# Kernel tuning notes

Hardware: AMD Instinct MI355X
Metric: run time of the kernel (lower is better)

The kernel has to match this reference:

```python
import jax, jax.numpy as jnp
import numpy as np

U = 128  # linear_units

def setup_inputs() -> dict:
    key = jax.random.key(0)
    k1, k2, k3, k4, k5, k6 = jax.random.split(key, 6)
    B, S, D = 16, 2048, 128
    x = jax.random.normal(k1, (B, S, D), dtype=jnp.float32)
    t = jax.random.uniform(k2, (B, S), dtype=jnp.float32)
    # glorot_uniform inits
    lim_qk = np.sqrt(6.0 / (D + U)).astype(np.float32)
    Wq = jax.random.uniform(k3, (D, U), minval=-lim_qk, maxval=lim_qk, dtype=jnp.float32)
    Wk = jax.random.uniform(k4, (D, U), minval=-lim_qk, maxval=lim_qk, dtype=jnp.float32)
    lim_s = np.sqrt(6.0 / (1 + S)).astype(np.float32)
    theta = jax.random.uniform(k5, (1, S), minval=-lim_s, maxval=lim_s, dtype=jnp.float32)
    mu = jax.random.uniform(k6, (1, S), minval=-lim_s, maxval=lim_s, dtype=jnp.float32)
    return {"x": x, "t": t, "Wq": Wq, "Wk": Wk, "theta": theta, "mu": mu}

def reference(x, t, Wq, Wk, theta, mu):
    # x: (B,S,D), t: (B,S), theta/mu: (1,S)
    scale = jnp.sqrt(jnp.asarray(U, dtype=x.dtype))
    q = x @ Wq                                   # (B,S,U)
    k = x @ Wk                                   # (B,S,U)
    scores = jnp.einsum('biu,bju->bij', q, k) / scale  # (B,S,S)
    alphas = jax.nn.softmax(scores, axis=-1)
    gn = jnp.einsum('bij,bjd->bid', alphas, x)   # weighted sum == alphas @ x, (B,S,D)
    time_fact = jax.nn.sigmoid(theta - mu * t)   # (B,S)
    v = jnp.sum(gn * time_fact[:, :, None], axis=1)  # (B,D)
    return v
```

## Files before the change

kernel.cpp:

```cpp
#include <hip/hip_runtime.h>
#include <hip/hip_bf16.h>

#define SS 2048
#define DD 128
#define BB 16
#define LDST 136
#define SCT 268

typedef short bf16x8 __attribute__((ext_vector_type(8)));
typedef float f32x4 __attribute__((ext_vector_type(4)));
typedef unsigned short ushort_t;

__device__ __forceinline__ unsigned short f2bf(float f) {
  union { float f; unsigned u; } v; v.f = f;
  unsigned r = v.u + 0x7fffu + ((v.u >> 16) & 1u);
  return (unsigned short)(r >> 16);
}
__device__ __forceinline__ float fexp2(float x) { return __builtin_amdgcn_exp2f(x); }


__global__ __launch_bounds__(256) void wprep(
    const float* __restrict__ Wq, const float* __restrict__ Wk,
    ushort_t* __restrict__ wt_g) {
  int idx = blockIdx.x * 256 + threadIdx.x;
  int r = idx & 16383, uu = r >> 7, d = r & 127;
  if (idx < 16384)
    wt_g[uu * 128 + d] = f2bf(Wq[d * 128 + uu] * 0.1275174346f);
  else
    wt_g[(uu + 128) * 128 + d] = f2bf(Wk[d * 128 + uu]);
}

__global__ __launch_bounds__(256, 2) void qk_gemm(
    const float* __restrict__ x, const ushort_t* __restrict__ wt_g,
    uint4* __restrict__ qF, uint4* __restrict__ kF) {
  __shared__ ushort_t xs[64 * LDST];
  __shared__ ushort_t sc[64 * SCT];
  const int tid = threadIdx.x, wave = tid >> 6, lane = tid & 63;
  const int lq = lane & 15, quad = lane >> 4;
  const int m0 = blockIdx.x * 64;

#pragma unroll
  for (int i = 0; i < 8; ++i) {
    int idx = i * 256 + tid;
    int row = idx >> 5, c4 = (idx & 31) * 4;
    const float4 v = *(const float4*)(x + (size_t)(m0 + row) * DD + c4);
    ushort4 h;
    h.x = f2bf(v.x); h.y = f2bf(v.y); h.z = f2bf(v.z); h.w = f2bf(v.w);
    *(ushort4*)(&xs[row * LDST + c4]) = h;
  }
  bf16x8 wf[4][4];
#pragma unroll
  for (int nt = 0; nt < 4; ++nt)
#pragma unroll
    for (int ks = 0; ks < 4; ++ks)
      wf[nt][ks] = *(const bf16x8*)(wt_g + (wave * 64 + nt * 16 + lq) * 128 + ks * 32 + quad * 8);
  __syncthreads();

  f32x4 acc[4][4];
#pragma unroll
  for (int mt = 0; mt < 4; ++mt)
#pragma unroll
    for (int nt = 0; nt < 4; ++nt) acc[mt][nt] = (f32x4){0.f, 0.f, 0.f, 0.f};
#pragma unroll
  for (int mt = 0; mt < 4; ++mt) {
    bf16x8 af[4];
#pragma unroll
    for (int ks = 0; ks < 4; ++ks)
      af[ks] = *(const bf16x8*)(&xs[(mt * 16 + lq) * LDST + ks * 32 + quad * 8]);
#pragma unroll
    for (int nt = 0; nt < 4; ++nt)
#pragma unroll
      for (int ks = 0; ks < 4; ++ks)
        acc[mt][nt] = __builtin_amdgcn_mfma_f32_16x16x32_bf16(af[ks], wf[nt][ks], acc[mt][nt], 0, 0, 0);
  }
#pragma unroll
  for (int mt = 0; mt < 4; ++mt)
#pragma unroll
    for (int nt = 0; nt < 4; ++nt)
#pragma unroll
      for (int r = 0; r < 4; ++r)
        sc[(mt * 16 + quad * 4 + r) * SCT + wave * 64 + nt * 16 + lq] = f2bf(acc[mt][nt][r]);
  __syncthreads();
#pragma unroll
  for (int i = 0; i < 8; ++i) {
    int c = i * 256 + tid;
    int lane_c = c & 63, ks_c = (c >> 6) & 3, g_c = (c >> 8) & 3, isk = c >> 10;
    int li = lane_c & 15, qd = lane_c >> 4;
    int col = isk * 128 + ks_c * 32 + qd * 8;
    uint4 v = *(const uint4*)(&sc[(g_c * 16 + li) * SCT + col]);
    size_t G = (size_t)blockIdx.x * 4 + g_c;
    uint4* dst = isk ? kF : qF;
    dst[(G * 4 + ks_c) * 64 + lane_c] = v;
  }
}

__global__ __launch_bounds__(256, 2) void attn_fused(
    const uint4* __restrict__ qF, const uint4* __restrict__ kF,
    const float* __restrict__ t, const float* __restrict__ theta,
    const float* __restrict__ mu, float* __restrict__ w) {
  const int b = blockIdx.x >> 5;
  const int ib = blockIdx.x & 31;
  const int i0 = ib * 64;
  const int tid = threadIdx.x, wave = tid >> 6, lane = tid & 63;
  const int lq = lane & 15, quad = lane >> 4;

  __shared__ float rs_lds[4][64];
  __shared__ float c_lds[64];

  const bf16x8* qc = (const bf16x8*)qF;
  const bf16x8* kc = (const bf16x8*)kF;

  bf16x8 af[4][4];
#pragma unroll
  for (int mt = 0; mt < 4; ++mt)
#pragma unroll
    for (int ks = 0; ks < 4; ++ks)
      af[mt][ks] = qc[((size_t)(b * 128 + ib * 4 + mt) * 4 + ks) * 64 + lane];

  bf16x8 cur[2][4], nxt[2][4];
  auto load_tile = [&](bf16x8 (&f)[2][4], int jt) {
#pragma unroll
    for (int nt = 0; nt < 2; ++nt) {
      int gg = jt * 8 + wave * 2 + nt;
#pragma unroll
      for (int ks = 0; ks < 4; ++ks)
        f[nt][ks] = kc[((size_t)(b * 128 + gg) * 4 + ks) * 64 + lane];
    }
  };

  float rowsum[4][4];
#pragma unroll
  for (int mt = 0; mt < 4; ++mt)
#pragma unroll
    for (int r = 0; r < 4; ++r) rowsum[mt][r] = 0.f;

  auto compute_p1 = [&](bf16x8 (&f)[2][4]) {
#pragma unroll
    for (int nt = 0; nt < 2; ++nt) {
      f32x4 acc[4];
#pragma unroll
      for (int mt = 0; mt < 4; ++mt) acc[mt] = (f32x4){0.f, 0.f, 0.f, 0.f};
#pragma unroll
      for (int ks = 0; ks < 4; ++ks)
#pragma unroll
        for (int mt = 0; mt < 4; ++mt)
          acc[mt] = __builtin_amdgcn_mfma_f32_16x16x32_bf16(af[mt][ks], f[nt][ks], acc[mt], 0, 0, 0);
#pragma unroll
      for (int mt = 0; mt < 4; ++mt)
#pragma unroll
        for (int r = 0; r < 4; ++r) rowsum[mt][r] += fexp2(acc[mt][r]);
    }
  };

  load_tile(cur, 0);
  for (int jt = 0; jt < 16; jt += 2) {
    load_tile(nxt, jt + 1);
    compute_p1(cur);
    if (jt + 2 < 16) load_tile(cur, jt + 2);
    compute_p1(nxt);
  }

#pragma unroll
  for (int d2 = 1; d2 <= 8; d2 <<= 1)
#pragma unroll
    for (int mt = 0; mt < 4; ++mt)
#pragma unroll
      for (int r = 0; r < 4; ++r)
        rowsum[mt][r] += __shfl_xor(rowsum[mt][r], d2, 64);
  if (lq == 0) {
#pragma unroll
    for (int mt = 0; mt < 4; ++mt)
#pragma unroll
      for (int r = 0; r < 4; ++r)
        rs_lds[wave][mt * 16 + quad * 4 + r] = rowsum[mt][r];
  }
  __syncthreads();
  if (tid < 64) {
    float l = rs_lds[0][tid] + rs_lds[1][tid] + rs_lds[2][tid] + rs_lds[3][tid];
    int gi = i0 + tid;
    float z = theta[gi] - mu[gi] * t[b * SS + gi];
    float tf = 1.f / (1.f + fexp2(-z * 1.44269504f));
    c_lds[tid] = tf / l;
  }
  __syncthreads();
  float creg[4][4];
#pragma unroll
  for (int mt = 0; mt < 4; ++mt)
#pragma unroll
    for (int r = 0; r < 4; ++r) creg[mt][r] = c_lds[mt * 16 + quad * 4 + r];

  auto compute_p2 = [&](bf16x8 (&f)[2][4], int jt) {
#pragma unroll
    for (int nt = 0; nt < 2; ++nt) {
      f32x4 acc[4];
#pragma unroll
      for (int mt = 0; mt < 4; ++mt) acc[mt] = (f32x4){0.f, 0.f, 0.f, 0.f};
#pragma unroll
      for (int ks = 0; ks < 4; ++ks)
#pragma unroll
        for (int mt = 0; mt < 4; ++mt)
          acc[mt] = __builtin_amdgcn_mfma_f32_16x16x32_bf16(af[mt][ks], f[nt][ks], acc[mt], 0, 0, 0);
      float cs = 0.f;
#pragma unroll
      for (int mt = 0; mt < 4; ++mt)
#pragma unroll
        for (int r = 0; r < 4; ++r) cs = fmaf(creg[mt][r], fexp2(acc[mt][r]), cs);
      cs += __shfl_xor(cs, 16, 64);
      cs += __shfl_xor(cs, 32, 64);
      if (lane < 16)
        atomicAdd(&w[b * SS + (jt * 8 + wave * 2 + nt) * 16 + lane], cs);
    }
  };

  load_tile(cur, 0);
  for (int jt = 0; jt < 16; jt += 2) {
    load_tile(nxt, jt + 1);
    compute_p2(cur, jt);
    if (jt + 2 < 16) load_tile(cur, jt + 2);
    compute_p2(nxt, jt + 1);
  }
}

__global__ __launch_bounds__(256) void finalize(
    const float* __restrict__ x, const float* __restrict__ w,
    float* __restrict__ out) {
  const int b = blockIdx.x >> 5;
  const int j0 = (blockIdx.x & 31) * 64;
  const int tid = threadIdx.x;
  const int d = tid & 127, jo = tid >> 7;
  float acc = 0.f;
  for (int jj = 0; jj < 32; ++jj) {
    int j = j0 + jj * 2 + jo;
    acc = fmaf(w[b * SS + j], x[((size_t)b * SS + j) * DD + d], acc);
  }
  __shared__ float red[256];
  red[tid] = acc;
  __syncthreads();
  if (tid < 128) atomicAdd(&out[b * DD + tid], red[tid] + red[tid + 128]);
}

extern "C" void kernel_launch(void* const* d_in, const int* in_sizes, int n_in,
                              void* d_out, int out_size, void* d_ws, size_t ws_size,
                              hipStream_t stream) {
  const float* x = (const float*)d_in[0];
  const float* t = (const float*)d_in[1];
  const float* Wq = (const float*)d_in[2];
  const float* Wk = (const float*)d_in[3];
  const float* theta = (const float*)d_in[4];
  const float* mu = (const float*)d_in[5];
  float* out = (float*)d_out;

  uint4* qF = (uint4*)d_ws;
  uint4* kF = qF + (size_t)2048 * 4 * 64;
  ushort_t* wt_g = (ushort_t*)(kF + (size_t)2048 * 4 * 64);
  float* w = (float*)(wt_g + 256 * 128);

  hipMemsetAsync(w, 0, (size_t)BB * SS * sizeof(float), stream);
  hipMemsetAsync(d_out, 0, (size_t)BB * DD * sizeof(float), stream);

  wprep<<<dim3(128), dim3(256), 0, stream>>>(Wq, Wk, wt_g);
  qk_gemm<<<dim3(512), dim3(256), 0, stream>>>(x, wt_g, qF, kF);
  attn_fused<<<dim3(512), dim3(256), 0, stream>>>(qF, kF, t, theta, mu, w);
  finalize<<<dim3(512), dim3(256), 0, stream>>>(x, w, out);
}
```

Baseline: 127.3 us.

## Split fused attention into two passes with key-split grid and atomic rowsums

Splits the fused attention kernel into pass1, cvec and pass2. pass1 computes softmax row sums, cvec computes the per-row coefficients, and pass2 applies them. Each pass splits the key dimension in two, doubling the grid to 1024 blocks, and raises launch bounds to 4 blocks per CU for more occupancy. Partial row sums are combined with global atomics. In exchange it adds two kernel launches and a memset, and drops the software prefetch double-buffering of key tiles.

Result: slower. 137.1 us (+7.7%).

```diff
diff --git a/kernel.cpp b/kernel.cpp
--- a/kernel.cpp
+++ b/kernel.cpp
@@ -94,18 +94,14 @@
   }
 }
 
-__global__ __launch_bounds__(256, 2) void attn_fused(
+__global__ __launch_bounds__(256, 4) void pass1(
     const uint4* __restrict__ qF, const uint4* __restrict__ kF,
-    const float* __restrict__ t, const float* __restrict__ theta,
-    const float* __restrict__ mu, float* __restrict__ w) {
-  const int b = blockIdx.x >> 5;
-  const int ib = blockIdx.x & 31;
+    float* __restrict__ l) {
+  const int blk = blockIdx.x;
+  const int jc = blk & 1, ib = (blk >> 1) & 31, b = blk >> 6;
   const int i0 = ib * 64;
   const int tid = threadIdx.x, wave = tid >> 6, lane = tid & 63;
-  const int lq = lane & 15, quad = lane >> 4;
-
-  __shared__ float rs_lds[4][64];
-  __shared__ float c_lds[64];
+  const int quad = lane >> 4;
 
   const bf16x8* qc = (const bf16x8*)qF;
   const bf16x8* kc = (const bf16x8*)kF;
@@ -117,49 +113,31 @@
     for (int ks = 0; ks < 4; ++ks)
       af[mt][ks] = qc[((size_t)(b * 128 + ib * 4 + mt) * 4 + ks) * 64 + lane];
 
-  bf16x8 cur[2][4], nxt[2][4];
-  auto load_tile = [&](bf16x8 (&f)[2][4], int jt) {
-#pragma unroll
-    for (int nt = 0; nt < 2; ++nt) {
-      int gg = jt * 8 + wave * 2 + nt;
-#pragma unroll
-      for (int ks = 0; ks < 4; ++ks)
-        f[nt][ks] = kc[((size_t)(b * 128 + gg) * 4 + ks) * 64 + lane];
-    }
-  };
-
   float rowsum[4][4];
 #pragma unroll
   for (int mt = 0; mt < 4; ++mt)
 #pragma unroll
     for (int r = 0; r < 4; ++r) rowsum[mt][r] = 0.f;
 
-  auto compute_p1 = [&](bf16x8 (&f)[2][4]) {
-#pragma unroll
-    for (int nt = 0; nt < 2; ++nt) {
-      f32x4 acc[4];
-#pragma unroll
-      for (int mt = 0; mt < 4; ++mt) acc[mt] = (f32x4){0.f, 0.f, 0.f, 0.f};
-#pragma unroll
-      for (int ks = 0; ks < 4; ++ks)
-#pragma unroll
-        for (int mt = 0; mt < 4; ++mt)
-          acc[mt] = __builtin_amdgcn_mfma_f32_16x16x32_bf16(af[mt][ks], f[nt][ks], acc[mt], 0, 0, 0);
+  for (int s = 0; s < 16; ++s) {
+    const int gg = b * 128 + jc * 64 + s * 4 + wave;
+    bf16x8 bf[4];
+#pragma unroll
+    for (int ks = 0; ks < 4; ++ks)
+      bf[ks] = kc[((size_t)gg * 4 + ks) * 64 + lane];
+    f32x4 acc[4];
+#pragma unroll
+    for (int mt = 0; mt < 4; ++mt) acc[mt] = (f32x4){0.f, 0.f, 0.f, 0.f};
+#pragma unroll
+    for (int ks = 0; ks < 4; ++ks)
 #pragma unroll
       for (int mt = 0; mt < 4; ++mt)
-#pragma unroll
-        for (int r = 0; r < 4; ++r) rowsum[mt][r] += fexp2(acc[mt][r]);
-    }
-  };
-
-  load_tile(cur, 0);
-  for (int jt = 0; jt < 16; jt += 2) {
-    load_tile(nxt, jt + 1);
-    compute_p1(cur);
-    if (jt + 2 < 16) load_tile(cur, jt + 2);
-    compute_p1(nxt);
-  }
-
+        acc[mt] = __builtin_amdgcn_mfma_f32_16x16x32_bf16(af[mt][ks], bf[ks], acc[mt], 0, 0, 0);
+#pragma unroll
+    for (int mt = 0; mt < 4; ++mt)
+#pragma unroll
+      for (int r = 0; r < 4; ++r) rowsum[mt][r] += fexp2(acc[mt][r]);
+  }
 #pragma unroll
   for (int d2 = 1; d2 <= 8; d2 <<= 1)
 #pragma unroll
@@ -167,57 +145,76 @@
 #pragma unroll
       for (int r = 0; r < 4; ++r)
         rowsum[mt][r] += __shfl_xor(rowsum[mt][r], d2, 64);
-  if (lq == 0) {
+  if ((lane & 15) == 0) {
 #pragma unroll
     for (int mt = 0; mt < 4; ++mt)
 #pragma unroll
       for (int r = 0; r < 4; ++r)
-        rs_lds[wave][mt * 16 + quad * 4 + r] = rowsum[mt][r];
-  }
-  __syncthreads();
-  if (tid < 64) {
-    float l = rs_lds[0][tid] + rs_lds[1][tid] + rs_lds[2][tid] + rs_lds[3][tid];
-    int gi = i0 + tid;
-    float z = theta[gi] - mu[gi] * t[b * SS + gi];
-    float tf = 1.f / (1.f + fexp2(-z * 1.44269504f));
-    c_lds[tid] = tf / l;
-  }
-  __syncthreads();
+        atomicAdd(&l[b * SS + i0 + mt * 16 + quad * 4 + r], rowsum[mt][r]);
+  }
+}
+
+__global__ __launch_bounds__(256) void cvec(
+    const float* __restrict__ t, const float* __restrict__ theta,
+    const float* __restrict__ mu, const float* __restrict__ l,
+    float* __restrict__ c) {
+  int idx = blockIdx.x * 256 + threadIdx.x;
+  int i = idx & 2047;
+  float z = theta[i] - mu[i] * t[idx];
+  float tf = 1.f / (1.f + fexp2(-z * 1.44269504f));
+  c[idx] = tf / l[idx];
+}
+
+__global__ __launch_bounds__(256, 4) void pass2(
+    const uint4* __restrict__ qF, const uint4* __restrict__ kF,
+    const float* __restrict__ c, float* __restrict__ w) {
+  const int blk = blockIdx.x;
+  const int jc = blk & 1, ib = (blk >> 1) & 31, b = blk >> 6;
+  const int i0 = ib * 64;
+  const int tid = threadIdx.x, wave = tid >> 6, lane = tid & 63;
+  const int quad = lane >> 4;
+
+  const bf16x8* qc = (const bf16x8*)qF;
+  const bf16x8* kc = (const bf16x8*)kF;
+
+  bf16x8 af[4][4];
+#pragma unroll
+  for (int mt = 0; mt < 4; ++mt)
+#pragma unroll
+    for (int ks = 0; ks < 4; ++ks)
+      af[mt][ks] = qc[((size_t)(b * 128 + ib * 4 + mt) * 4 + ks) * 64 + lane];
+
   float creg[4][4];
 #pragma unroll
   for (int mt = 0; mt < 4; ++mt)
 #pragma unroll
-    for (int r = 0; r < 4; ++r) creg[mt][r] = c_lds[mt * 16 + quad * 4 + r];
-
-  auto compute_p2 = [&](bf16x8 (&f)[2][4], int jt) {
-#pragma unroll
-    for (int nt = 0; nt < 2; ++nt) {
-      f32x4 acc[4];
-#pragma unroll
-      for (int mt = 0; mt < 4; ++mt) acc[mt] = (f32x4){0.f, 0.f, 0.f, 0.f};
-#pragma unroll
-      for (int ks = 0; ks < 4; ++ks)
-#pragma unroll
-        for (int mt = 0; mt < 4; ++mt)
-          acc[mt] = __builtin_amdgcn_mfma_f32_16x16x32_bf16(af[mt][ks], f[nt][ks], acc[mt], 0, 0, 0);
-      float cs = 0.f;
+    for (int r = 0; r < 4; ++r)
+      creg[mt][r] = c[b * SS + i0 + mt * 16 + quad * 4 + r];
+
+  for (int s = 0; s < 16; ++s) {
+    const int ggl = jc * 64 + s * 4 + wave;
+    const int gg = b * 128 + ggl;
+    bf16x8 bf[4];
+#pragma unroll
+    for (int ks = 0; ks < 4; ++ks)
+      bf[ks] = kc[((size_t)gg * 4 + ks) * 64 + lane];
+    f32x4 acc[4];
+#pragma unroll
+    for (int mt = 0; mt < 4; ++mt) acc[mt] = (f32x4){0.f, 0.f, 0.f, 0.f};
+#pragma unroll
+    for (int ks = 0; ks < 4; ++ks)
 #pragma unroll
       for (int mt = 0; mt < 4; ++mt)
-#pragma unroll
-        for (int r = 0; r < 4; ++r) cs = fmaf(creg[mt][r], fexp2(acc[mt][r]), cs);
-      cs += __shfl_xor(cs, 16, 64);
-      cs += __shfl_xor(cs, 32, 64);
-      if (lane < 16)
-        atomicAdd(&w[b * SS + (jt * 8 + wave * 2 + nt) * 16 + lane], cs);
-    }
-  };
-
-  load_tile(cur, 0);
-  for (int jt = 0; jt < 16; jt += 2) {
-    load_tile(nxt, jt + 1);
-    compute_p2(cur, jt);
-    if (jt + 2 < 16) load_tile(cur, jt + 2);
-    compute_p2(nxt, jt + 1);
+        acc[mt] = __builtin_amdgcn_mfma_f32_16x16x32_bf16(af[mt][ks], bf[ks], acc[mt], 0, 0, 0);
+    float cs = 0.f;
+#pragma unroll
+    for (int mt = 0; mt < 4; ++mt)
+#pragma unroll
+      for (int r = 0; r < 4; ++r) cs = fmaf(creg[mt][r], fexp2(acc[mt][r]), cs);
+    cs += __shfl_xor(cs, 16, 64);
+    cs += __shfl_xor(cs, 32, 64);
+    if (lane < 16)
+      atomicAdd(&w[b * SS + ggl * 16 + lane], cs);
   }
 }
 
@@ -253,13 +250,18 @@
   uint4* qF = (uint4*)d_ws;
   uint4* kF = qF + (size_t)2048 * 4 * 64;
   ushort_t* wt_g = (ushort_t*)(kF + (size_t)2048 * 4 * 64);
-  float* w = (float*)(wt_g + 256 * 128);
-
+  float* l = (float*)(wt_g + 256 * 128);
+  float* c = l + (size_t)BB * SS;
+  float* w = c + (size_t)BB * SS;
+
+  hipMemsetAsync(l, 0, (size_t)BB * SS * sizeof(float), stream);
   hipMemsetAsync(w, 0, (size_t)BB * SS * sizeof(float), stream);
   hipMemsetAsync(d_out, 0, (size_t)BB * DD * sizeof(float), stream);
 
   wprep<<<dim3(128), dim3(256), 0, stream>>>(Wq, Wk, wt_g);
   qk_gemm<<<dim3(512), dim3(256), 0, stream>>>(x, wt_g, qF, kF);
-  attn_fused<<<dim3(512), dim3(256), 0, stream>>>(qF, kF, t, theta, mu, w);
+  pass1<<<dim3(1024), dim3(256), 0, stream>>>(qF, kF, l);
+  cvec<<<dim3(128), dim3(256), 0, stream>>>(t, theta, mu, l, c);
+  pass2<<<dim3(1024), dim3(256), 0, stream>>>(qF, kF, c, w);
   finalize<<<dim3(512), dim3(256), 0, stream>>>(x, w, out);
 }
```
